# Kernel optimization log

Hardware: AMD Instinct MI355X
Metric: run time of the kernel (lower is better)

## Reference

```python
import jax, jax.numpy as jnp
import numpy as np

H = 51  # num_hidden

def lstm_cell(x, h, c, Wih, Whh, bih, bhh):
    # PyTorch LSTMCell gate order: i, f, g, o
    gates = x @ Wih.T + bih + h @ Whh.T + bhh
    i, f, g, o = jnp.split(gates, 4, axis=-1)
    c_new = jax.nn.sigmoid(f) * c + jax.nn.sigmoid(i) * jnp.tanh(g)
    h_new = jax.nn.sigmoid(o) * jnp.tanh(c_new)
    return h_new, c_new

def setup_inputs() -> dict:
    key = jax.random.key(0)
    ks = jax.random.split(key, 9)
    B, T = 8192, 512
    s1 = 1.0 / np.sqrt(H)  # torch LSTMCell init scale U(-1/sqrt(H), 1/sqrt(H))
    s2 = 1.0
    u = lambda k, shape, s: jax.random.uniform(k, shape, jnp.float32, -s, s)
    return {
        "x": jax.random.normal(ks[0], (B, T), dtype=jnp.float32),
        "Wih1": u(ks[1], (4 * H, 1), s1),
        "Whh1": u(ks[2], (4 * H, H), s1),
        "bih1": u(ks[3], (4 * H,), s1),
        "bhh1": u(ks[4], (4 * H,), s1),
        "Wih2": u(ks[5], (4, H), s2),
        "Whh2": u(ks[6], (4, 1), s2),
        "bih2": u(ks[7], (4,), s2),
        "bhh2": u(ks[8], (4,), s2),
    }

def reference(x, Wih1, Whh1, bih1, bhh1, Wih2, Whh2, bih2, bhh2):
    B, T = x.shape
    xs = x.T[:, :, None]  # [T, B, 1]
    h1 = jnp.zeros((B, H), x.dtype)
    c1 = jnp.zeros((B, H), x.dtype)
    h2 = jnp.zeros((B, 1), x.dtype)
    c2 = jnp.zeros((B, 1), x.dtype)

    def step(carry, xt):
        h1, c1, h2, c2 = carry
        h1, c1 = lstm_cell(xt, h1, c1, Wih1, Whh1, bih1, bhh1)
        h2, c2 = lstm_cell(c1, h2, c2, Wih2, Whh2, bih2, bhh2)
        return (h1, c1, h2, c2), None

    (h1, c1, h2, c2), _ = jax.lax.scan(step, (h1, c1, h2, c2), xs)
    # extra step after the loop (as in the original forward)
    h1, c1 = lstm_cell(c2, h1, c1, Wih1, Whh1, bih1, bhh1)
    h2, output = lstm_cell(c1, h2, c2, Wih2, Whh2, bih2, bhh2)
    return output  # [B, 1] (final cell state of lstm2)
```

## Files before the change

### kernel.cpp

```cpp
#include <hip/hip_runtime.h>

#define TT 512
#define L2E  1.4426950408889634f
#define L2E2 2.8853900817779268f

typedef _Float16 f16;
typedef _Float16 f16x8 __attribute__((ext_vector_type(8)));
typedef float f32x4 __attribute__((ext_vector_type(4)));

__device__ __forceinline__ float fsig_p(float a){
    return __builtin_amdgcn_rcpf(1.f + __builtin_amdgcn_exp2f(-a));
}
__device__ __forceinline__ float ftanhg_p(float a){
    return 2.f * __builtin_amdgcn_rcpf(1.f + __builtin_amdgcn_exp2f(-a)) - 1.f;
}
__device__ __forceinline__ float ftanh_c(float c){
    return 2.f * __builtin_amdgcn_rcpf(1.f + __builtin_amdgcn_exp2f(-L2E2*c)) - 1.f;
}

#define FMA_LO(accv, wd, hh) asm("v_fma_mix_f32 %0, %1, %2, %0 op_sel:[0,0,0] op_sel_hi:[1,0,0]" : "+v"(accv) : "v"(wd), "v"(hh))
#define FMA_HI(accv, wd, hh) asm("v_fma_mix_f32 %0, %1, %2, %0 op_sel:[1,0,0] op_sel_hi:[1,0,0]" : "+v"(accv) : "v"(wd), "v"(hh))

__global__ void repack_w(const float* __restrict__ Whh1, const float* __restrict__ Wih1,
                         const float* __restrict__ bih1, const float* __restrict__ bhh1,
                         const float* __restrict__ Wih2,
                         f16* __restrict__ Wp, f16* __restrict__ Wp2)
{
    int i = blockIdx.x*256 + threadIdx.x;
    if (i < 13*2*64*8) {
        int b    = i & 7;
        int lane = (i >> 3) & 63;
        int kt   = (i >> 9) & 1;
        int m    = i >> 10;
        int r = m*16 + (lane & 15);
        int u = r >> 2, g = r & 3;
        int k = kt*32 + (lane >> 4)*8 + b;
        float v = 0.f;
        if (u < 51) {
            int rt = g*51 + u;
            if      (k < 51)  v = Whh1[rt*51 + k];
            else if (k == 51) v = Wih1[rt];
            else if (k == 52) v = bih1[rt] + bhh1[rt];
            v *= (g == 2) ? L2E2 : L2E;
        }
        Wp[i] = (f16)v;
    }
    if (i < 224) {
        int u = i >> 2, g = i & 3;
        float v = (u < 51) ? Wih2[g*51 + u] : 0.f;
        v *= (g == 2) ? L2E2 : L2E;
        Wp2[i] = (f16)v;
    }
}

__global__ __launch_bounds__(256, 2) void lstm_main(
    const float* __restrict__ X, const f16* __restrict__ Wp, const f16* __restrict__ Wp2,
    const float* __restrict__ Whh2, const float* __restrict__ bih2, const float* __restrict__ bhh2,
    float* __restrict__ out)
{
    __shared__ __align__(16) f16   HB[1024];
    __shared__ __align__(16) float PBL[4][16][4];

    const int tid  = threadIdx.x;
    const int w    = tid >> 6;
    const int lane = tid & 63;
    const int q    = (lane >> 4) & 3;
    const int jl   = lane & 15;
    const int d8   = jl & 7;
    const int bb   = blockIdx.x * 16;

    if (w == 1 || w == 3) __builtin_amdgcn_s_setprio(1);

    for (int i = tid; i < 512; i += 256) ((unsigned*)HB)[i] = 0u;
    if (tid < 256) ((unsigned*)PBL)[tid] = 0u;
    __syncthreads();
    if (w == 0 && lane < 16) {
        int dd = lane & 7;
        HB[lane*64 + ((6 ^ dd) << 3) + 4] = (f16)1.f;
        HB[lane*64 + ((6 ^ dd) << 3) + 3] = (f16)X[(size_t)(bb + lane)*TT];
    }

    const bool has4 = (w == 1);
    const int tiles[4] = {w, 4+w, 8+w, 12};
    f16x8 A0[4], A1[4];
    uint2 w2p[4];
    #pragma unroll
    for (int k = 0; k < 4; ++k) {
        int m = tiles[k];
        A0[k]  = *(const f16x8*)(Wp + (m*2+0)*512 + lane*8);
        A1[k]  = *(const f16x8*)(Wp + (m*2+1)*512 + lane*8);
        w2p[k] = *(const uint2*)(Wp2 + (m*4+q)*4);
    }
    float wh2[4], bs2[4];
    #pragma unroll
    for (int g = 0; g < 4; ++g) {
        float sc = (g == 2) ? L2E2 : L2E;
        wh2[g] = Whh2[g] * sc;
        bs2[g] = (bih2[g] + bhh2[g]) * sc;
    }

    float c1[4] = {0.f, 0.f, 0.f, 0.f};
    float c2 = 0.f, h2 = 0.f;
    const f32x4 zero4 = {0.f, 0.f, 0.f, 0.f};

    const float* xp = X + (size_t)(bb + jl) * TT;
    __syncthreads();

    for (int t = 0; t < TT; ++t) {
        const f16* rb = HB + jl*64;
        f16x8 B0 = *(const f16x8*)(rb + ((q       ^ d8) << 3));
        f16x8 B1 = *(const f16x8*)(rb + (((4 + q) ^ d8) << 3));

        f32x4 S0, S1, S2, S3;
        if (w == 3) {
            S0 = *(const f32x4*)&PBL[0][jl][0];
            S1 = *(const f32x4*)&PBL[1][jl][0];
            S2 = *(const f32x4*)&PBL[2][jl][0];
            S3 = *(const f32x4*)&PBL[3][jl][0];
        }
        float xn = 0.f;
        if (w == 0) xn = xp[(t+1 < TT) ? t+1 : t];

        __syncthreads();

        if (w == 3 && t > 0) {
            f32x4 S = S0 + S1 + S2 + S3;
            float g0 = S[0] + bs2[0] + wh2[0]*h2;
            float g1 = S[1] + bs2[1] + wh2[1]*h2;
            float g2 = S[2] + bs2[2] + wh2[2]*h2;
            float g3 = S[3] + bs2[3] + wh2[3]*h2;
            float i2 = fsig_p(g0), f2 = fsig_p(g1), gg2 = ftanhg_p(g2), o2 = fsig_p(g3);
            c2 = f2*c2 + i2*gg2;
            h2 = o2*ftanh_c(c2);
        }

        float p0 = 0.f, p1 = 0.f, p2 = 0.f, p3 = 0.f;
        #pragma unroll
        for (int k = 0; k < 4; ++k) {
            if (k < 3 || has4) {
                f32x4 a = __builtin_amdgcn_mfma_f32_16x16x32_f16(A0[k], B0, zero4, 0,0,0);
                a       = __builtin_amdgcn_mfma_f32_16x16x32_f16(A1[k], B1, a,     0,0,0);
                float ig = fsig_p(a[0]), fg = fsig_p(a[1]), gg = ftanhg_p(a[2]), og = fsig_p(a[3]);
                float c  = fg*c1[k] + ig*gg;
                c1[k] = c;
                int u = tiles[k]*4 + q;
                if (k < 3 || q < 3)
                    HB[jl*64 + (((u >> 3) ^ d8) << 3) + (u & 7)] = (f16)(og * ftanh_c(c));
                FMA_LO(p0, w2p[k].x, c); FMA_HI(p1, w2p[k].x, c);
                FMA_LO(p2, w2p[k].y, c); FMA_HI(p3, w2p[k].y, c);
            }
        }
        if (w == 0 && q == 3)
            HB[jl*64 + ((6 ^ d8) << 3) + 3] = (f16)xn;

        p0 += __shfl_xor(p0, 16); p0 += __shfl_xor(p0, 32);
        p1 += __shfl_xor(p1, 16); p1 += __shfl_xor(p1, 32);
        p2 += __shfl_xor(p2, 16); p2 += __shfl_xor(p2, 32);
        p3 += __shfl_xor(p3, 16); p3 += __shfl_xor(p3, 32);
        if (lane < 16) {
            f32x4 pv = {p0, p1, p2, p3};
            *(f32x4*)&PBL[w][jl][0] = pv;
        }
        __syncthreads();
    }

    if (w == 3) {
        f32x4 S = *(const f32x4*)&PBL[0][jl][0];
        S += *(const f32x4*)&PBL[1][jl][0];
        S += *(const f32x4*)&PBL[2][jl][0];
        S += *(const f32x4*)&PBL[3][jl][0];
        float g0 = S[0] + bs2[0] + wh2[0]*h2;
        float g1 = S[1] + bs2[1] + wh2[1]*h2;
        float g2 = S[2] + bs2[2] + wh2[2]*h2;
        float g3 = S[3] + bs2[3] + wh2[3]*h2;
        float i2 = fsig_p(g0), f2 = fsig_p(g1), gg2 = ftanhg_p(g2), o2 = fsig_p(g3);
        c2 = f2*c2 + i2*gg2;
        h2 = o2*ftanh_c(c2);
        if (lane < 16) HB[jl*64 + ((6 ^ d8) << 3) + 3] = (f16)c2;
    }
    __syncthreads();

    {
        const f16* rb = HB + jl*64;
        f16x8 B0 = *(const f16x8*)(rb + ((q       ^ d8) << 3));
        f16x8 B1 = *(const f16x8*)(rb + (((4 + q) ^ d8) << 3));

        float p0 = 0.f, p1 = 0.f, p2 = 0.f, p3 = 0.f;
        #pragma unroll
        for (int k = 0; k < 4; ++k) {
            if (k < 3 || has4) {
                f32x4 a = __builtin_amdgcn_mfma_f32_16x16x32_f16(A0[k], B0, zero4, 0,0,0);
                a       = __builtin_amdgcn_mfma_f32_16x16x32_f16(A1[k], B1, a,     0,0,0);
                float ig = fsig_p(a[0]), fg = fsig_p(a[1]), gg = ftanhg_p(a[2]);
                float c  = fg*c1[k] + ig*gg;
                FMA_LO(p0, w2p[k].x, c); FMA_HI(p1, w2p[k].x, c);
                FMA_LO(p2, w2p[k].y, c); FMA_HI(p3, w2p[k].y, c);
            }
        }
        p0 += __shfl_xor(p0, 16); p0 += __shfl_xor(p0, 32);
        p1 += __shfl_xor(p1, 16); p1 += __shfl_xor(p1, 32);
        p2 += __shfl_xor(p2, 16); p2 += __shfl_xor(p2, 32);
        p3 += __shfl_xor(p3, 16); p3 += __shfl_xor(p3, 32);
        if (lane < 16) {
            f32x4 pv = {p0, p1, p2, p3};
            *(f32x4*)&PBL[w][jl][0] = pv;
        }
    }
    __syncthreads();

    if (w == 3) {
        f32x4 S = *(const f32x4*)&PBL[0][jl][0];
        S += *(const f32x4*)&PBL[1][jl][0];
        S += *(const f32x4*)&PBL[2][jl][0];
        S += *(const f32x4*)&PBL[3][jl][0];
        float g0 = S[0] + bs2[0] + wh2[0]*h2;
        float g1 = S[1] + bs2[1] + wh2[1]*h2;
        float g2 = S[2] + bs2[2] + wh2[2]*h2;
        float i2 = fsig_p(g0), f2 = fsig_p(g1), gg2 = ftanhg_p(g2);
        float c2n = f2*c2 + i2*gg2;
        if (lane < 16) out[bb + jl] = c2n;
    }
}

extern "C" void kernel_launch(void* const* d_in, const int* in_sizes, int n_in,
                              void* d_out, int out_size, void* d_ws, size_t ws_size,
                              hipStream_t stream) {
    const float* X    = (const float*)d_in[0];
    const float* Wih1 = (const float*)d_in[1];
    const float* Whh1 = (const float*)d_in[2];
    const float* bih1 = (const float*)d_in[3];
    const float* bhh1 = (const float*)d_in[4];
    const float* Wih2 = (const float*)d_in[5];
    const float* Whh2 = (const float*)d_in[6];
    const float* bih2 = (const float*)d_in[7];
    const float* bhh2 = (const float*)d_in[8];
    float* out = (float*)d_out;

    f16* Wp  = (f16*)d_ws;
    f16* Wp2 = (f16*)((char*)d_ws + 26624);

    repack_w<<<52, 256, 0, stream>>>(Whh1, Wih1, bih1, bhh1, Wih2, Wp, Wp2);
    lstm_main<<<512, 256, 0, stream>>>(X, Wp, Wp2, Whh2, bih2, bhh2, out);
}
```

Before: 461.3 us.

## Interleave two independent 16-row batches per block and preload X into LDS

Each block now handles 32 batch rows as two independent 16-row groups with separate LDS state buffers. The block alternates phases: it reads one group's buffers while computing the other, so the two recurrences overlap and one group's dependency latency can be hidden behind the other's work. The whole input slice is also loaded once into LDS as f16, which removes the per-step global load of x. Grid size drops to 256 blocks with launch bounds of 1 block per CU, trading occupancy and registers for this interleaving. The final step also stops writing the unused fourth gate partial.

```diff
diff --git a/kernel.cpp b/kernel.cpp
--- a/kernel.cpp
+++ b/kernel.cpp
@@ -53,13 +53,69 @@
     }
 }
 
-__global__ __launch_bounds__(256, 2) void lstm_main(
+#define RD_PHASE(HBg, PBLg, rowoff, tn, B0v, B1v, S0v, S1v, S2v, S3v, xnv) do {  \
+    const f16* rb_ = (HBg) + jl*64;                                              \
+    B0v = *(const f16x8*)(rb_ + ((q       ^ d8) << 3));                          \
+    B1v = *(const f16x8*)(rb_ + (((4 + q) ^ d8) << 3));                          \
+    if (w == 3) {                                                                \
+        S0v = *(const f32x4*)&(PBLg)[0][jl][0];                                  \
+        S1v = *(const f32x4*)&(PBLg)[1][jl][0];                                  \
+        S2v = *(const f32x4*)&(PBLg)[2][jl][0];                                  \
+        S3v = *(const f32x4*)&(PBLg)[3][jl][0];                                  \
+    }                                                                            \
+    if (w == 0) xnv = HX[(tn)*32 + (rowoff) + jl];                               \
+} while (0)
+
+#define WR_PHASE(doL2, HBg, PBLg, B0v, B1v, S0v, S1v, S2v, S3v, xnv, c1v, c2v, h2v) do { \
+    if (w == 3 && (doL2)) {                                                      \
+        f32x4 Ss_ = S0v + S1v + S2v + S3v;                                       \
+        float g0_ = Ss_[0] + bs2[0] + wh2[0]*h2v;                                \
+        float g1_ = Ss_[1] + bs2[1] + wh2[1]*h2v;                                \
+        float g2_ = Ss_[2] + bs2[2] + wh2[2]*h2v;                                \
+        float g3_ = Ss_[3] + bs2[3] + wh2[3]*h2v;                                \
+        float i2_ = fsig_p(g0_), f2_ = fsig_p(g1_);                              \
+        float gg2_ = ftanhg_p(g2_), o2_ = fsig_p(g3_);                           \
+        c2v = f2_*c2v + i2_*gg2_;                                                \
+        h2v = o2_*ftanh_c(c2v);                                                  \
+    }                                                                            \
+    float p0_ = 0.f, p1_ = 0.f, p2_ = 0.f, p3_ = 0.f;                            \
+    _Pragma("unroll")                                                            \
+    for (int k_ = 0; k_ < 4; ++k_) {                                             \
+        if (k_ < 3 || has4) {                                                    \
+            f32x4 a_ = __builtin_amdgcn_mfma_f32_16x16x32_f16(A0[k_], B0v, zero4, 0,0,0); \
+            a_       = __builtin_amdgcn_mfma_f32_16x16x32_f16(A1[k_], B1v, a_,    0,0,0); \
+            float ig_ = fsig_p(a_[0]), fg_ = fsig_p(a_[1]);                      \
+            float gg_ = ftanhg_p(a_[2]), og_ = fsig_p(a_[3]);                    \
+            float c_ = fg_*c1v[k_] + ig_*gg_;                                    \
+            c1v[k_] = c_;                                                        \
+            int u_ = tiles[k_]*4 + q;                                            \
+            if (k_ < 3 || q < 3)         \
+                (HBg)[jl*64 + (((u_>>3) ^ d8) << 3) + (u_&7)] = (f16)(og_*ftanh_c(c_)); \
+            FMA_LO(p0_, w2p[k_].x, c_); FMA_HI(p1_, w2p[k_].x, c_);              \
+            FMA_LO(p2_, w2p[k_].y, c_); FMA_HI(p3_, w2p[k_].y, c_);              \
+        }                                                                        \
+    }                                                                            \
+    if (w == 0 && q == 3) (HBg)[jl*64 + ((6 ^ d8) << 3) + 3] = xnv;              \
+    p0_ += __shfl_xor(p0_, 16); p0_ += __shfl_xor(p0_, 32);                      \
+    p1_ += __shfl_xor(p1_, 16); p1_ += __shfl_xor(p1_, 32);                      \
+    p2_ += __shfl_xor(p2_, 16); p2_ += __shfl_xor(p2_, 32);                      \
+    p3_ += __shfl_xor(p3_, 16); p3_ += __shfl_xor(p3_, 32);                      \
+    if (lane < 16) {                                                             \
+        f32x4 pv_ = {p0_, p1_, p2_, p3_};                                        \
+        *(f32x4*)&(PBLg)[w][jl][0] = pv_;                                        \
+    }                                                                            \
+} while (0)
+
+__global__ __launch_bounds__(256, 1) void lstm_main(
     const float* __restrict__ X, const f16* __restrict__ Wp, const f16* __restrict__ Wp2,
     const float* __restrict__ Whh2, const float* __restrict__ bih2, const float* __restrict__ bhh2,
     float* __restrict__ out)
 {
-    __shared__ __align__(16) f16   HB[1024];
-    __shared__ __align__(16) float PBL[4][16][4];
+    __shared__ __align__(16) f16   HBA[1024];
+    __shared__ __align__(16) f16   HBB[1024];
+    __shared__ __align__(16) float PBLA[4][16][4];
+    __shared__ __align__(16) float PBLB[4][16][4];
+    __shared__ __align__(16) f16   HX[TT*32];
 
     const int tid  = threadIdx.x;
     const int w    = tid >> 6;
@@ -67,21 +123,32 @@
     const int q    = (lane >> 4) & 3;
     const int jl   = lane & 15;
     const int d8   = jl & 7;
-    const int bb   = blockIdx.x * 16;
-
-    if (w == 1 || w == 3) __builtin_amdgcn_s_setprio(1);
-
-    for (int i = tid; i < 512; i += 256) ((unsigned*)HB)[i] = 0u;
-    if (tid < 256) ((unsigned*)PBL)[tid] = 0u;
+    const int bb32 = blockIdx.x * 32;
+
+    for (int i = tid; i < 512; i += 256) { ((unsigned*)HBA)[i] = 0u; ((unsigned*)HBB)[i] = 0u; }
+    { ((unsigned*)PBLA)[tid] = 0u; ((unsigned*)PBLB)[tid] = 0u; }
+
+    #pragma unroll
+    for (int it = 0; it < 16; ++it) {
+        int flat = it*1024 + tid*4;
+        int row = flat >> 9, col = flat & 511;
+        float4 v = *(const float4*)(X + (size_t)(bb32 + row)*TT + col);
+        HX[(col+0)*32 + row] = (f16)v.x;
+        HX[(col+1)*32 + row] = (f16)v.y;
+        HX[(col+2)*32 + row] = (f16)v.z;
+        HX[(col+3)*32 + row] = (f16)v.w;
+    }
     __syncthreads();
     if (w == 0 && lane < 16) {
         int dd = lane & 7;
-        HB[lane*64 + ((6 ^ dd) << 3) + 4] = (f16)1.f;
-        HB[lane*64 + ((6 ^ dd) << 3) + 3] = (f16)X[(size_t)(bb + lane)*TT];
+        HBA[lane*64 + ((6 ^ dd) << 3) + 4] = (f16)1.f;
+        HBB[lane*64 + ((6 ^ dd) << 3) + 4] = (f16)1.f;
+        HBA[lane*64 + ((6 ^ dd) << 3) + 3] = HX[0*32 + lane];
+        HBB[lane*64 + ((6 ^ dd) << 3) + 3] = HX[0*32 + 16 + lane];
     }
 
     const bool has4 = (w == 1);
-    const int tiles[4] = {w, 4+w, 8+w, 12};
+    const int tiles[4] = { w, 4+w, 8+w, 12 };
     f16x8 A0[4], A1[4];
     uint2 w2p[4];
     #pragma unroll
@@ -99,126 +166,138 @@
         bs2[g] = (bih2[g] + bhh2[g]) * sc;
     }
 
-    float c1[4] = {0.f, 0.f, 0.f, 0.f};
-    float c2 = 0.f, h2 = 0.f;
+    float c1A[4] = {0.f,0.f,0.f,0.f}, c1B[4] = {0.f,0.f,0.f,0.f};
+    float c2A = 0.f, h2A = 0.f, c2B = 0.f, h2B = 0.f;
     const f32x4 zero4 = {0.f, 0.f, 0.f, 0.f};
 
-    const float* xp = X + (size_t)(bb + jl) * TT;
+    f16x8 B0A = {}, B1A = {}, B0B = {}, B1B = {};
+    f32x4 SA0 = zero4, SA1 = zero4, SA2 = zero4, SA3 = zero4;
+    f32x4 SB0 = zero4, SB1 = zero4, SB2 = zero4, SB3 = zero4;
+    f16 xnA = (f16)0.f, xnB = (f16)0.f;
+
+    __syncthreads();
+
+    RD_PHASE(HBA, PBLA, 0, 1, B0A, B1A, SA0, SA1, SA2, SA3, xnA);
     __syncthreads();
 
     for (int t = 0; t < TT; ++t) {
-        const f16* rb = HB + jl*64;
-        f16x8 B0 = *(const f16x8*)(rb + ((q       ^ d8) << 3));
-        f16x8 B1 = *(const f16x8*)(rb + (((4 + q) ^ d8) << 3));
-
-        f32x4 S0, S1, S2, S3;
-        if (w == 3) {
-            S0 = *(const f32x4*)&PBL[0][jl][0];
-            S1 = *(const f32x4*)&PBL[1][jl][0];
-            S2 = *(const f32x4*)&PBL[2][jl][0];
-            S3 = *(const f32x4*)&PBL[3][jl][0];
-        }
-        float xn = 0.f;
-        if (w == 0) xn = xp[(t+1 < TT) ? t+1 : t];
-
-        __syncthreads();
-
-        if (w == 3 && t > 0) {
-            f32x4 S = S0 + S1 + S2 + S3;
-            float g0 = S[0] + bs2[0] + wh2[0]*h2;
-            float g1 = S[1] + bs2[1] + wh2[1]*h2;
-            float g2 = S[2] + bs2[2] + wh2[2]*h2;
-            float g3 = S[3] + bs2[3] + wh2[3]*h2;
+        {
+            const int tnB = (t+1 < TT) ? t+1 : TT-1;
+            RD_PHASE(HBB, PBLB, 16, tnB, B0B, B1B, SB0, SB1, SB2, SB3, xnB);
+            WR_PHASE(t > 0, HBA, PBLA, B0A, B1A, SA0, SA1, SA2, SA3, xnA, c1A, c2A, h2A);
+            __syncthreads();
+        }
+        {
+            const int tnA = (t+2 < TT) ? t+2 : TT-1;
+            RD_PHASE(HBA, PBLA, 0, tnA, B0A, B1A, SA0, SA1, SA2, SA3, xnA);
+            WR_PHASE(t > 0, HBB, PBLB, B0B, B1B, SB0, SB1, SB2, SB3, xnB, c1B, c2B, h2B);
+            __syncthreads();
+        }
+    }
+
+    if (w == 3) {
+        {
+            f32x4 Ss = SA0 + SA1 + SA2 + SA3;
+            float g0 = Ss[0] + bs2[0] + wh2[0]*h2A;
+            float g1 = Ss[1] + bs2[1] + wh2[1]*h2A;
+            float g2 = Ss[2] + bs2[2] + wh2[2]*h2A;
+            float g3 = Ss[3] + bs2[3] + wh2[3]*h2A;
             float i2 = fsig_p(g0), f2 = fsig_p(g1), gg2 = ftanhg_p(g2), o2 = fsig_p(g3);
-            c2 = f2*c2 + i2*gg2;
-            h2 = o2*ftanh_c(c2);
-        }
-
-        float p0 = 0.f, p1 = 0.f, p2 = 0.f, p3 = 0.f;
+            c2A = f2*c2A + i2*gg2;
+            h2A = o2*ftanh_c(c2A);
+        }
+        {
+            f32x4 Ss = *(const f32x4*)&PBLB[0][jl][0];
+            Ss += *(const f32x4*)&PBLB[1][jl][0];
+            Ss += *(const f32x4*)&PBLB[2][jl][0];
+            Ss += *(const f32x4*)&PBLB[3][jl][0];
+            float g0 = Ss[0] + bs2[0] + wh2[0]*h2B;
+            float g1 = Ss[1] + bs2[1] + wh2[1]*h2B;
+            float g2 = Ss[2] + bs2[2] + wh2[2]*h2B;
+            float g3 = Ss[3] + bs2[3] + wh2[3]*h2B;
+            float i2 = fsig_p(g0), f2 = fsig_p(g1), gg2 = ftanhg_p(g2), o2 = fsig_p(g3);
+            c2B = f2*c2B + i2*gg2;
+            h2B = o2*ftanh_c(c2B);
+        }
+        if (lane < 16) {
+            int dd = lane & 7;
+            HBA[lane*64 + ((6 ^ dd) << 3) + 3] = (f16)c2A;
+            HBB[lane*64 + ((6 ^ dd) << 3) + 3] = (f16)c2B;
+        }
+    }
+    __syncthreads();
+
+    {
+        const f16* rbA = HBA + jl*64;
+        const f16* rbB = HBB + jl*64;
+        f16x8 b0a = *(const f16x8*)(rbA + ((q       ^ d8) << 3));
+        f16x8 b1a = *(const f16x8*)(rbA + (((4 + q) ^ d8) << 3));
+        f16x8 b0b = *(const f16x8*)(rbB + ((q       ^ d8) << 3));
+        f16x8 b1b = *(const f16x8*)(rbB + (((4 + q) ^ d8) << 3));
+
+        float pA0=0.f, pA1=0.f, pA2=0.f, pA3=0.f;
+        float pB0=0.f, pB1=0.f, pB2=0.f, pB3=0.f;
         #pragma unroll
         for (int k = 0; k < 4; ++k) {
             if (k < 3 || has4) {
-                f32x4 a = __builtin_amdgcn_mfma_f32_16x16x32_f16(A0[k], B0, zero4, 0,0,0);
-                a       = __builtin_amdgcn_mfma_f32_16x16x32_f16(A1[k], B1, a,     0,0,0);
-                float ig = fsig_p(a[0]), fg = fsig_p(a[1]), gg = ftanhg_p(a[2]), og = fsig_p(a[3]);
-                float c  = fg*c1[k] + ig*gg;
-                c1[k] = c;
-                int u = tiles[k]*4 + q;
-                if (k < 3 || q < 3)
-                    HB[jl*64 + (((u >> 3) ^ d8) << 3) + (u & 7)] = (f16)(og * ftanh_c(c));
-                FMA_LO(p0, w2p[k].x, c); FMA_HI(p1, w2p[k].x, c);
-                FMA_LO(p2, w2p[k].y, c); FMA_HI(p3, w2p[k].y, c);
+                f32x4 aA = __builtin_amdgcn_mfma_f32_16x16x32_f16(A0[k], b0a, zero4, 0,0,0);
+                aA       = __builtin_amdgcn_mfma_f32_16x16x32_f16(A1[k], b1a, aA,    0,0,0);
+                f32x4 aB = __builtin_amdgcn_mfma_f32_16x16x32_f16(A0[k], b0b, zero4, 0,0,0);
+                aB       = __builtin_amdgcn_mfma_f32_16x16x32_f16(A1[k], b1b, aB,    0,0,0);
+                {
+                    float ig = fsig_p(aA[0]), fg = fsig_p(aA[1]), gg = ftanhg_p(aA[2]);
+                    float c  = fg*c1A[k] + ig*gg;
+                    FMA_LO(pA0, w2p[k].x, c); FMA_HI(pA1, w2p[k].x, c);
+                    FMA_LO(pA2, w2p[k].y, c); FMA_HI(pA3, w2p[k].y, c);
+                }
+                {
+                    float ig = fsig_p(aB[0]), fg = fsig_p(aB[1]), gg = ftanhg_p(aB[2]);
+                    float c  = fg*c1B[k] + ig*gg;
+                    FMA_LO(pB0, w2p[k].x, c); FMA_HI(pB1, w2p[k].x, c);
+                    FMA_LO(pB2, w2p[k].y, c); FMA_HI(pB3, w2p[k].y, c);
+                }
             }
         }
-        if (w == 0 && q == 3)
-            HB[jl*64 + ((6 ^ d8) << 3) + 3] = (f16)xn;
-
-        p0 += __shfl_xor(p0, 16); p0 += __shfl_xor(p0, 32);
-        p1 += __shfl_xor(p1, 16); p1 += __shfl_xor(p1, 32);
-        p2 += __shfl_xor(p2, 16); p2 += __shfl_xor(p2, 32);
-        p3 += __shfl_xor(p3, 16); p3 += __shfl_xor(p3, 32);
+        pA0 += __shfl_xor(pA0, 16); pA0 += __shfl_xor(pA0, 32);
+        pA1 += __shfl_xor(pA1, 16); pA1 += __shfl_xor(pA1, 32);
+        pA2 += __shfl_xor(pA2, 16); pA2 += __shfl_xor(pA2, 32);
+        pB0 += __shfl_xor(pB0, 16); pB0 += __shfl_xor(pB0, 32);
+        pB1 += __shfl_xor(pB1, 16); pB1 += __shfl_xor(pB1, 32);
+        pB2 += __shfl_xor(pB2, 16); pB2 += __shfl_xor(pB2, 32);
         if (lane < 16) {
-            f32x4 pv = {p0, p1, p2, p3};
-            *(f32x4*)&PBL[w][jl][0] = pv;
-        }
-        __syncthreads();
-    }
+            f32x4 pa = {pA0, pA1, pA2, 0.f};
+            f32x4 pb = {pB0, pB1, pB2, 0.f};
+            *(f32x4*)&PBLA[w][jl][0] = pa;
+            *(f32x4*)&PBLB[w][jl][0] = pb;
+        }
+    }
+    __syncthreads();
 
     if (w == 3) {
-        f32x4 S = *(const f32x4*)&PBL[0][jl][0];
-        S += *(const f32x4*)&PBL[1][jl][0];
-        S += *(const f32x4*)&PBL[2][jl][0];
-        S += *(const f32x4*)&PBL[3][jl][0];
-        float g0 = S[0] + bs2[0] + wh2[0]*h2;
-        float g1 = S[1] + bs2[1] + wh2[1]*h2;
-        float g2 = S[2] + bs2[2] + wh2[2]*h2;
-        float g3 = S[3] + bs2[3] + wh2[3]*h2;
-        float i2 = fsig_p(g0), f2 = fsig_p(g1), gg2 = ftanhg_p(g2), o2 = fsig_p(g3);
-        c2 = f2*c2 + i2*gg2;
-        h2 = o2*ftanh_c(c2);
-        if (lane < 16) HB[jl*64 + ((6 ^ d8) << 3) + 3] = (f16)c2;
-    }
-    __syncthreads();
-
-    {
-        const f16* rb = HB + jl*64;
-        f16x8 B0 = *(const f16x8*)(rb + ((q       ^ d8) << 3));
-        f16x8 B1 = *(const f16x8*)(rb + (((4 + q) ^ d8) << 3));
-
-        float p0 = 0.f, p1 = 0.f, p2 = 0.f, p3 = 0.f;
-        #pragma unroll
-        for (int k = 0; k < 4; ++k) {
-            if (k < 3 || has4) {
-                f32x4 a = __builtin_amdgcn_mfma_f32_16x16x32_f16(A0[k], B0, zero4, 0,0,0);
-                a       = __builtin_amdgcn_mfma_f32_16x16x32_f16(A1[k], B1, a,     0,0,0);
-                float ig = fsig_p(a[0]), fg = fsig_p(a[1]), gg = ftanhg_p(a[2]);
-                float c  = fg*c1[k] + ig*gg;
-                FMA_LO(p0, w2p[k].x, c); FMA_HI(p1, w2p[k].x, c);
-                FMA_LO(p2, w2p[k].y, c); FMA_HI(p3, w2p[k].y, c);
-            }
-        }
-        p0 += __shfl_xor(p0, 16); p0 += __shfl_xor(p0, 32);
-        p1 += __shfl_xor(p1, 16); p1 += __shfl_xor(p1, 32);
-        p2 += __shfl_xor(p2, 16); p2 += __shfl_xor(p2, 32);
-        p3 += __shfl_xor(p3, 16); p3 += __shfl_xor(p3, 32);
-        if (lane < 16) {
-            f32x4 pv = {p0, p1, p2, p3};
-            *(f32x4*)&PBL[w][jl][0] = pv;
-        }
-    }
-    __syncthreads();
-
-    if (w == 3) {
-        f32x4 S = *(const f32x4*)&PBL[0][jl][0];
-        S += *(const f32x4*)&PBL[1][jl][0];
-        S += *(const f32x4*)&PBL[2][jl][0];
-        S += *(const f32x4*)&PBL[3][jl][0];
-        float g0 = S[0] + bs2[0] + wh2[0]*h2;
-        float g1 = S[1] + bs2[1] + wh2[1]*h2;
-        float g2 = S[2] + bs2[2] + wh2[2]*h2;
-        float i2 = fsig_p(g0), f2 = fsig_p(g1), gg2 = ftanhg_p(g2);
-        float c2n = f2*c2 + i2*gg2;
-        if (lane < 16) out[bb + jl] = c2n;
+        {
+            f32x4 Ss = *(const f32x4*)&PBLA[0][jl][0];
+            Ss += *(const f32x4*)&PBLA[1][jl][0];
+            Ss += *(const f32x4*)&PBLA[2][jl][0];
+            Ss += *(const f32x4*)&PBLA[3][jl][0];
+            float g0 = Ss[0] + bs2[0] + wh2[0]*h2A;
+            float g1 = Ss[1] + bs2[1] + wh2[1]*h2A;
+            float g2 = Ss[2] + bs2[2] + wh2[2]*h2A;
+            float i2 = fsig_p(g0), f2 = fsig_p(g1), gg2 = ftanhg_p(g2);
+            float c2n = f2*c2A + i2*gg2;
+            if (lane < 16) out[bb32 + jl] = c2n;
+        }
+        {
+            f32x4 Ss = *(const f32x4*)&PBLB[0][jl][0];
+            Ss += *(const f32x4*)&PBLB[1][jl][0];
+            Ss += *(const f32x4*)&PBLB[2][jl][0];
+            Ss += *(const f32x4*)&PBLB[3][jl][0];
+            float g0 = Ss[0] + bs2[0] + wh2[0]*h2B;
+            float g1 = Ss[1] + bs2[1] + wh2[1]*h2B;
+            float g2 = Ss[2] + bs2[2] + wh2[2]*h2B;
+            float i2 = fsig_p(g0), f2 = fsig_p(g1), gg2 = ftanhg_p(g2);
+            float c2n = f2*c2B + i2*gg2;
+            if (lane < 16) out[bb32 + 16 + jl] = c2n;
+        }
     }
 }
 
@@ -240,5 +319,5 @@
     f16* Wp2 = (f16*)((char*)d_ws + 26624);
 
     repack_w<<<52, 256, 0, stream>>>(Whh1, Wih1, bih1, bhh1, Wih2, Wp, Wp2);
-    lstm_main<<<512, 256, 0, stream>>>(X, Wp, Wp2, Whh2, bih2, bhh2, out);
-}
+    lstm_main<<<256, 256, 0, stream>>>(X, Wp, Wp2, Whh2, bih2, bhh2, out);
+}
```

Measured after the change: 630.4 us. +36.7%, slower.
